# Performance work log

Hardware: AMD Instinct MI355X
Metric: run time of the kernel (lower is better)

The kernel has to match this reference:

```python
import jax, jax.numpy as jnp
import numpy as np

NUM_ADAPTIVE = 8
WEIGHT_ALPHA = 1.0


def setup_inputs() -> dict:
    key = jax.random.key(0)
    k1, k2, k3, k4 = jax.random.split(key, 4)
    B, C, S = 128, 4, 65536
    inp = jax.random.normal(k1, (B, C, S), dtype=jnp.float32)
    target = jax.random.randint(k2, (B, S), 0, C, dtype=jnp.int64)
    adaptive_target = jax.random.randint(k3, (B, S), 0, NUM_ADAPTIVE, dtype=jnp.int64)
    mask = jax.random.randint(k4, (B, S), 0, 2).astype(jnp.float32)
    return {"input": inp, "target": target, "adaptive_target": adaptive_target, "mask": mask}


def reference(input, target, adaptive_target, mask):
    # Per-position cross entropy, reduction='none'. input: (B, C, S)
    logp = jax.nn.log_softmax(input, axis=1)                      # (B, C, S)
    ce = -jnp.take_along_axis(logp, target[:, None, :], axis=1)[:, 0, :]  # (B, S)

    loss = ce * mask                                              # masked per-position loss
    valid = (mask > 0).astype(loss.dtype)                         # (B, S)

    # Per-adaptive-class masked mean loss via a single segment reduction
    seg = adaptive_target.reshape(-1).astype(jnp.int32)
    class_sum = jax.ops.segment_sum((loss * valid).reshape(-1), seg, num_segments=NUM_ADAPTIVE)
    class_cnt = jax.ops.segment_sum(valid.reshape(-1), seg, num_segments=NUM_ADAPTIVE)

    fallback = jnp.mean(loss)                                     # loss.mean() in the original
    has = class_cnt > 0
    class_losses = jnp.where(has, class_sum / jnp.where(has, class_cnt, 1.0), fallback)
    class_counts = jnp.where(has, class_cnt, 1.0)

    total = jnp.sum(class_losses * class_counts)
    props = jnp.where(total > 0,
                      class_losses * class_counts / jnp.where(total > 0, total, 1.0),
                      jnp.full((NUM_ADAPTIVE,), 1.0 / NUM_ADAPTIVE, dtype=loss.dtype))
    class_weights = 1.0 + WEIGHT_ALPHA * props                    # (8,)

    adaptive_weights = class_weights[adaptive_target]             # gather back to (B, S)
    final_loss = jnp.sum(loss * adaptive_weights) / jnp.sum(mask)
    return final_loss
```

## Files before the change

### kernel.cpp

```cpp
#include <hip/hip_runtime.h>

constexpr int B = 128;
constexpr int C = 4;
constexpr int S = 65536;
constexpr int N = B * S;
constexpr int NG = N / 4;
constexpr int NSEG = 8;
constexpr int NACC = 2 * NSEG;

constexpr int GRID  = 512;
constexpr int BLOCK = 256;
constexpr int WAVES = BLOCK / 64;
constexpr int NWAVE = GRID * WAVES;
constexpr int TILES = NG / (NWAVE * 64);
static_assert(TILES * NWAVE * 64 == NG, "exact tiling");

constexpr int SEGB  = 1024;
constexpr int TILEB = 7 * SEGB;
constexpr int DEPTH = 2;

typedef float fx4 __attribute__((ext_vector_type(4)));
typedef int   ix4 __attribute__((ext_vector_type(4)));

#define GLB(p) ((const __attribute__((address_space(1))) void*)(p))
#define LDS(p) ((__attribute__((address_space(3))) void*)(p))

__device__ __forceinline__ void issue_tile(
    const float* __restrict__ input, const int* __restrict__ target,
    const int* __restrict__ seg, const float* __restrict__ mask,
    char* lb, int wave_id, int t, int lane)
{
    const int g0 = (wave_id + t * NWAVE) * 64;
    const int p0 = g0 << 2;
    const int b  = p0 >> 16;
    const int s  = p0 & (S - 1);
    const int base = (b << 18) + s;
    const int lo = lane * 16;

    __builtin_amdgcn_global_load_lds(GLB((const char*)(input + base)         + lo), LDS(lb + 0 * SEGB), 16, 0, 0);
    __builtin_amdgcn_global_load_lds(GLB((const char*)(input + base +     S) + lo), LDS(lb + 1 * SEGB), 16, 0, 0);
    __builtin_amdgcn_global_load_lds(GLB((const char*)(input + base + 2 * S) + lo), LDS(lb + 2 * SEGB), 16, 0, 0);
    __builtin_amdgcn_global_load_lds(GLB((const char*)(input + base + 3 * S) + lo), LDS(lb + 3 * SEGB), 16, 0, 0);
    __builtin_amdgcn_global_load_lds(GLB((const char*)(target + p0)          + lo), LDS(lb + 4 * SEGB), 16, 0, 0);
    __builtin_amdgcn_global_load_lds(GLB((const char*)(seg    + p0)          + lo), LDS(lb + 5 * SEGB), 16, 0, 0);
    __builtin_amdgcn_global_load_lds(GLB((const char*)(mask   + p0)          + lo), LDS(lb + 6 * SEGB), 16, 0, 0);
}

__global__ __launch_bounds__(BLOCK) void ce_partial_kernel(
    const float* __restrict__ input,
    const int*   __restrict__ target,
    const int*   __restrict__ seg,
    const float* __restrict__ mask,
    float* __restrict__ pt)
{
    __shared__ __align__(16) char smem[WAVES * DEPTH * TILEB];
    __shared__ float red[WAVES][NACC];

    const int lane = threadIdx.x & 63;
    const int w    = threadIdx.x >> 6;
    const int wave_id = blockIdx.x * WAVES + w;
    char* mybuf = smem + w * (DEPTH * TILEB);

    float ssum[NSEG], scnt[NSEG];
#pragma unroll
    for (int k = 0; k < NSEG; ++k) { ssum[k] = 0.f; scnt[k] = 0.f; }

    issue_tile(input, target, seg, mask, mybuf, wave_id, 0, lane);

#pragma unroll 1
    for (int t = 0; t < TILES; ++t) {
        if (t + 1 < TILES) {
            issue_tile(input, target, seg, mask,
                       mybuf + ((t + 1) & 1) * TILEB, wave_id, t + 1, lane);
            asm volatile("s_waitcnt vmcnt(7)" ::: "memory");
        } else {
            asm volatile("s_waitcnt vmcnt(0)" ::: "memory");
        }

        const char* lb = mybuf + (t & 1) * TILEB;
        const int lo = lane * 16;
        const fx4 l0 = *(const fx4*)(lb + 0 * SEGB + lo);
        const fx4 l1 = *(const fx4*)(lb + 1 * SEGB + lo);
        const fx4 l2 = *(const fx4*)(lb + 2 * SEGB + lo);
        const fx4 l3 = *(const fx4*)(lb + 3 * SEGB + lo);
        const ix4 tg = *(const ix4*)(lb + 4 * SEGB + lo);
        const ix4 sv = *(const ix4*)(lb + 5 * SEGB + lo);
        const fx4 mk = *(const fx4*)(lb + 6 * SEGB + lo);

        const float a0[4] = { l0.x, l0.y, l0.z, l0.w };
        const float a1[4] = { l1.x, l1.y, l1.z, l1.w };
        const float a2[4] = { l2.x, l2.y, l2.z, l2.w };
        const float a3[4] = { l3.x, l3.y, l3.z, l3.w };
        const int   tgv[4] = { tg.x, tg.y, tg.z, tg.w };
        const int   sgv[4] = { sv.x, sv.y, sv.z, sv.w };
        const float mkv[4] = { mk.x, mk.y, mk.z, mk.w };

#pragma unroll
        for (int j = 0; j < 4; ++j) {
            const float x0 = a0[j], x1 = a1[j], x2 = a2[j], x3 = a3[j];
            const float m = fmaxf(fmaxf(x0, x1), fmaxf(x2, x3));
            const float sum = __expf(x0 - m) + __expf(x1 - m)
                            + __expf(x2 - m) + __expf(x3 - m);
            const float lse = m + __logf(sum);
            const int tt = tgv[j];
            const float chosen = (tt == 0) ? x0 : (tt == 1) ? x1 : (tt == 2) ? x2 : x3;
            const float mval = mkv[j];
            const float loss = (lse - chosen) * mval;
            const int sgj = sgv[j];
#pragma unroll
            for (int k = 0; k < NSEG; ++k) {
                const bool hit = (sgj == k);
                ssum[k] += hit ? loss : 0.f;
                scnt[k] += hit ? mval : 0.f;
            }
        }
    }

    float vals[NACC];
#pragma unroll
    for (int k = 0; k < NSEG; ++k) { vals[k] = ssum[k]; vals[NSEG + k] = scnt[k]; }
#pragma unroll
    for (int i = 0; i < NACC; ++i) {
        float v = vals[i];
#pragma unroll
        for (int off = 32; off > 0; off >>= 1)
            v += __shfl_xor(v, off, 64);
        vals[i] = v;
    }

    if (lane == 0) {
#pragma unroll
        for (int i = 0; i < NACC; ++i) red[w][i] = vals[i];
    }
    __syncthreads();
    if (threadIdx.x < NACC) {
        const int i = threadIdx.x;
        pt[i * GRID + blockIdx.x] =
            red[0][i] + red[1][i] + red[2][i] + red[3][i];
    }
}

__global__ __launch_bounds__(512) void ce_final_kernel(
    const float* __restrict__ pt, float* __restrict__ out)
{
    const int t = threadIdx.x;
    float vals[NACC];
#pragma unroll
    for (int i = 0; i < NACC; ++i) {
        float v = pt[i * GRID + t];
#pragma unroll
        for (int off = 32; off > 0; off >>= 1)
            v += __shfl_xor(v, off, 64);
        vals[i] = v;
    }

    __shared__ float red[8][NACC];
    const int wave = t >> 6;
    const int lane = t & 63;
    if (lane == 0) {
#pragma unroll
        for (int i = 0; i < NACC; ++i) red[wave][i] = vals[i];
    }
    __syncthreads();

    if (t == 0) {
        float acc[NACC];
        for (int i = 0; i < NACC; ++i) {
            float v = 0.f;
            for (int w = 0; w < 8; ++w) v += red[w][i];
            acc[i] = v;
        }

        float ssum[NSEG], scnt[NSEG];
        float tot_loss = 0.f, msum = 0.f;
        for (int k = 0; k < NSEG; ++k) {
            ssum[k] = acc[k];
            scnt[k] = acc[NSEG + k];
            tot_loss += ssum[k];
            msum += scnt[k];
        }
        const float fallback = tot_loss / (float)N;

        float cl[NSEG], cc[NSEG];
        float total = 0.f;
        for (int k = 0; k < NSEG; ++k) {
            const bool has = scnt[k] > 0.f;
            cl[k] = has ? (ssum[k] / scnt[k]) : fallback;
            cc[k] = has ? scnt[k] : 1.f;
            total += cl[k] * cc[k];
        }
        float num = 0.f;
        for (int k = 0; k < NSEG; ++k) {
            const float prop = (total > 0.f) ? (cl[k] * cc[k] / total)
                                             : (1.f / (float)NSEG);
            const float w = 1.f + prop;
            num += w * ssum[k];
        }
        out[0] = num / msum;
    }
}

extern "C" void kernel_launch(void* const* d_in, const int* in_sizes, int n_in,
                              void* d_out, int out_size, void* d_ws, size_t ws_size,
                              hipStream_t stream) {
    const float* input  = (const float*)d_in[0];
    const int*   target = (const int*)d_in[1];
    const int*   seg    = (const int*)d_in[2];
    const float* mask   = (const float*)d_in[3];
    float* pt  = (float*)d_ws;
    float* out = (float*)d_out;

    ce_partial_kernel<<<GRID, BLOCK, 0, stream>>>(input, target, seg, mask, pt);
    ce_final_kernel<<<1, 512, 0, stream>>>(pt, out);
}
```

Before: 264.1 us.

## Load small per-position arrays into registers, double grid, use nontemporal loads

The target, segment and mask streams no longer go through LDS via global_load_lds. They are fetched with nontemporal vector loads straight into registers one tile ahead, which shrinks the per-wave LDS tile from seven segments to four. The logit loads into LDS also get the nontemporal cache-policy bit. The grid doubles to 1024 blocks, and the final reduction kernel grows to 1024 threads to match. The aim is higher occupancy and less LDS traffic for this streaming reduction. The risk is that the compiler's own waitcnt placement for the register prefetch interferes with the hand-written vmcnt(7) pipelining.

```diff
diff --git a/kernel.cpp b/kernel.cpp
--- a/kernel.cpp
+++ b/kernel.cpp
@@ -8,7 +8,7 @@
 constexpr int NSEG = 8;
 constexpr int NACC = 2 * NSEG;
 
-constexpr int GRID  = 512;
+constexpr int GRID  = 1024;
 constexpr int BLOCK = 256;
 constexpr int WAVES = BLOCK / 64;
 constexpr int NWAVE = GRID * WAVES;
@@ -16,7 +16,8 @@
 static_assert(TILES * NWAVE * 64 == NG, "exact tiling");
 
 constexpr int SEGB  = 1024;
-constexpr int TILEB = 7 * SEGB;
+constexpr int LSEG  = 4;
+constexpr int TILEB = LSEG * SEGB;
 constexpr int DEPTH = 2;
 
 typedef float fx4 __attribute__((ext_vector_type(4)));
@@ -25,7 +26,11 @@
 #define GLB(p) ((const __attribute__((address_space(1))) void*)(p))
 #define LDS(p) ((__attribute__((address_space(3))) void*)(p))
 
-__device__ __forceinline__ void issue_tile(
+constexpr int AUX_NT = 2;
+
+struct Sml { ix4 tg, sv; fx4 mk; };
+
+__device__ __forceinline__ Sml issue_tile(
     const float* __restrict__ input, const int* __restrict__ target,
     const int* __restrict__ seg, const float* __restrict__ mask,
     char* lb, int wave_id, int t, int lane)
@@ -37,13 +42,17 @@
     const int base = (b << 18) + s;
     const int lo = lane * 16;
 
-    __builtin_amdgcn_global_load_lds(GLB((const char*)(input + base)         + lo), LDS(lb + 0 * SEGB), 16, 0, 0);
-    __builtin_amdgcn_global_load_lds(GLB((const char*)(input + base +     S) + lo), LDS(lb + 1 * SEGB), 16, 0, 0);
-    __builtin_amdgcn_global_load_lds(GLB((const char*)(input + base + 2 * S) + lo), LDS(lb + 2 * SEGB), 16, 0, 0);
-    __builtin_amdgcn_global_load_lds(GLB((const char*)(input + base + 3 * S) + lo), LDS(lb + 3 * SEGB), 16, 0, 0);
-    __builtin_amdgcn_global_load_lds(GLB((const char*)(target + p0)          + lo), LDS(lb + 4 * SEGB), 16, 0, 0);
-    __builtin_amdgcn_global_load_lds(GLB((const char*)(seg    + p0)          + lo), LDS(lb + 5 * SEGB), 16, 0, 0);
-    __builtin_amdgcn_global_load_lds(GLB((const char*)(mask   + p0)          + lo), LDS(lb + 6 * SEGB), 16, 0, 0);
+    __builtin_amdgcn_global_load_lds(GLB((const char*)(input + base)         + lo), LDS(lb + 0 * SEGB), 16, 0, AUX_NT);
+    __builtin_amdgcn_global_load_lds(GLB((const char*)(input + base +     S) + lo), LDS(lb + 1 * SEGB), 16, 0, AUX_NT);
+    __builtin_amdgcn_global_load_lds(GLB((const char*)(input + base + 2 * S) + lo), LDS(lb + 2 * SEGB), 16, 0, AUX_NT);
+    __builtin_amdgcn_global_load_lds(GLB((const char*)(input + base + 3 * S) + lo), LDS(lb + 3 * SEGB), 16, 0, AUX_NT);
+
+    Sml r;
+    const int pp = p0 + (lane << 2);
+    r.tg = __builtin_nontemporal_load((const ix4*)(target + pp));
+    r.sv = __builtin_nontemporal_load((const ix4*)(seg + pp));
+    r.mk = __builtin_nontemporal_load((const fx4*)(mask + pp));
+    return r;
 }
 
 __global__ __launch_bounds__(BLOCK) void ce_partial_kernel(
@@ -65,13 +74,14 @@
 #pragma unroll
     for (int k = 0; k < NSEG; ++k) { ssum[k] = 0.f; scnt[k] = 0.f; }
 
-    issue_tile(input, target, seg, mask, mybuf, wave_id, 0, lane);
+    Sml cur = issue_tile(input, target, seg, mask, mybuf, wave_id, 0, lane);
 
 #pragma unroll 1
     for (int t = 0; t < TILES; ++t) {
+        Sml nxt;
         if (t + 1 < TILES) {
-            issue_tile(input, target, seg, mask,
-                       mybuf + ((t + 1) & 1) * TILEB, wave_id, t + 1, lane);
+            nxt = issue_tile(input, target, seg, mask,
+                             mybuf + ((t + 1) & 1) * TILEB, wave_id, t + 1, lane);
             asm volatile("s_waitcnt vmcnt(7)" ::: "memory");
         } else {
             asm volatile("s_waitcnt vmcnt(0)" ::: "memory");
@@ -83,17 +93,14 @@
         const fx4 l1 = *(const fx4*)(lb + 1 * SEGB + lo);
         const fx4 l2 = *(const fx4*)(lb + 2 * SEGB + lo);
         const fx4 l3 = *(const fx4*)(lb + 3 * SEGB + lo);
-        const ix4 tg = *(const ix4*)(lb + 4 * SEGB + lo);
-        const ix4 sv = *(const ix4*)(lb + 5 * SEGB + lo);
-        const fx4 mk = *(const fx4*)(lb + 6 * SEGB + lo);
 
         const float a0[4] = { l0.x, l0.y, l0.z, l0.w };
         const float a1[4] = { l1.x, l1.y, l1.z, l1.w };
         const float a2[4] = { l2.x, l2.y, l2.z, l2.w };
         const float a3[4] = { l3.x, l3.y, l3.z, l3.w };
-        const int   tgv[4] = { tg.x, tg.y, tg.z, tg.w };
-        const int   sgv[4] = { sv.x, sv.y, sv.z, sv.w };
-        const float mkv[4] = { mk.x, mk.y, mk.z, mk.w };
+        const int   tgv[4] = { cur.tg.x, cur.tg.y, cur.tg.z, cur.tg.w };
+        const int   sgv[4] = { cur.sv.x, cur.sv.y, cur.sv.z, cur.sv.w };
+        const float mkv[4] = { cur.mk.x, cur.mk.y, cur.mk.z, cur.mk.w };
 
 #pragma unroll
         for (int j = 0; j < 4; ++j) {
@@ -114,6 +121,7 @@
                 scnt[k] += hit ? mval : 0.f;
             }
         }
+        cur = nxt;
     }
 
     float vals[NACC];
@@ -140,7 +148,7 @@
     }
 }
 
-__global__ __launch_bounds__(512) void ce_final_kernel(
+__global__ __launch_bounds__(1024) void ce_final_kernel(
     const float* __restrict__ pt, float* __restrict__ out)
 {
     const int t = threadIdx.x;
@@ -154,7 +162,7 @@
         vals[i] = v;
     }
 
-    __shared__ float red[8][NACC];
+    __shared__ float red[16][NACC];
     const int wave = t >> 6;
     const int lane = t & 63;
     if (lane == 0) {
@@ -167,7 +175,7 @@
         float acc[NACC];
         for (int i = 0; i < NACC; ++i) {
             float v = 0.f;
-            for (int w = 0; w < 8; ++w) v += red[w][i];
+            for (int w = 0; w < 16; ++w) v += red[w][i];
             acc[i] = v;
         }
 
@@ -211,5 +219,5 @@
     float* out = (float*)d_out;
 
     ce_partial_kernel<<<GRID, BLOCK, 0, stream>>>(input, target, seg, mask, pt);
-    ce_final_kernel<<<1, 512, 0, stream>>>(pt, out);
-}
+    ce_final_kernel<<<1, 1024, 0, stream>>>(pt, out);
+}
```

New measurement: 247.8 us. -6.2%, faster.
